# Performance work log

Hardware: AMD Instinct MI355X
Metric: run time of the kernel (lower is better)

The kernel has to match this reference:

```python
import jax, jax.numpy as jnp
import numpy as np

B, LB, LWIN, CODE, H, LAYERS = 256, 4, 128, 64, 256, 2


def _lstm_layer(xs, h0, c0, Wih, Whh, b):
    # xs: [T, B, in]; returns hs [T, B, H], final (h, c)
    WihT, WhhT = Wih.T, Whh.T
    def step(carry, x_t):
        h, c = carry
        gates = x_t @ WihT + h @ WhhT + b  # [B, 4H]
        i, f, g, o = jnp.split(gates, 4, axis=-1)  # PyTorch gate order i,f,g,o
        i, f, o = jax.nn.sigmoid(i), jax.nn.sigmoid(f), jax.nn.sigmoid(o)
        g = jnp.tanh(g)
        c_new = f * c + i * g
        h_new = o * jnp.tanh(c_new)
        return (h_new, c_new), h_new
    (h_n, c_n), hs = jax.lax.scan(step, (h0, c0), xs)
    return hs, h_n, c_n


def _run_stack(xs, states, params):
    # xs: [T, B, in]; states: list of (h, c) per layer
    new_states = []
    for (Wih, Whh, bih, bhh), (h0, c0) in zip(params, states):
        xs, h_n, c_n = _lstm_layer(xs, h0, c0, Wih, Whh, bih + bhh)
        new_states.append((h_n, c_n))
    return xs, new_states


def setup_inputs() -> dict:
    key = jax.random.key(0)
    ks = jax.random.split(key, 12)
    s = 0.05
    return {
        "x": jax.random.normal(ks[0], (B, LB, LWIN, CODE), jnp.float32),
        "targets": jax.random.normal(ks[1], (B, LWIN, CODE), jnp.float32),
        "Wih_0": jax.random.normal(ks[2], (4 * H, CODE), jnp.float32) * s,
        "Whh_0": jax.random.normal(ks[3], (4 * H, H), jnp.float32) * s,
        "bih_0": jax.random.normal(ks[4], (4 * H,), jnp.float32) * s,
        "bhh_0": jax.random.normal(ks[5], (4 * H,), jnp.float32) * s,
        "Wih_1": jax.random.normal(ks[6], (4 * H, H), jnp.float32) * s,
        "Whh_1": jax.random.normal(ks[7], (4 * H, H), jnp.float32) * s,
        "bih_1": jax.random.normal(ks[8], (4 * H,), jnp.float32) * s,
        "bhh_1": jax.random.normal(ks[9], (4 * H,), jnp.float32) * s,
        "fcW": jax.random.normal(ks[10], (CODE, H), jnp.float32) * s,
        "fcb": jax.random.normal(ks[11], (CODE,), jnp.float32) * s,
    }


def reference(x, targets, Wih_0, Whh_0, bih_0, bhh_0, Wih_1, Whh_1, bih_1, bhh_1, fcW, fcb):
    params = [(Wih_0, Whh_0, bih_0, bhh_0), (Wih_1, Whh_1, bih_1, bhh_1)]
    b = x.shape[0]
    xe = x.reshape(b, LB * LWIN, CODE)  # (B, look_back*l_win, code)
    zeros = jnp.zeros((b, H), x.dtype)
    states = [(zeros, zeros) for _ in range(LAYERS)]
    # Encoder pass to get (h_n, c_n)
    _, states = _run_stack(jnp.swapaxes(xe, 0, 1), states, params)
    # Teacher-forced decoder: inputs are known upfront
    dec_in = jnp.concatenate([xe[:, -1:, :], targets[:, :-1, :]], axis=1)  # (B, l_win, code)
    dec_hs, _ = _run_stack(jnp.swapaxes(dec_in, 0, 1), states, params)  # (l_win, B, H)
    out = jnp.einsum('tbh,ch->btc', dec_hs, fcW) + fcb  # (B, l_win, code)
    return out
```

## Files before the change

### kernel.cpp

```cpp
#include <hip/hip_runtime.h>
#include <math.h>

#define BATCH  256
#define CODE   64
#define HID    256
#define TSTEPS 640
#define NGRP   16

#define OFF_A0   0
#define OFF_A1   327680
#define OFF_BP0  851968
#define OFF_BP1  852992
#define OFF_HEX  854016
#define WS_FLOATS (OFF_HEX + 524288)

typedef __attribute__((ext_vector_type(8))) short  short8;
typedef __attribute__((ext_vector_type(4))) float  f32x4;
typedef __attribute__((ext_vector_type(4))) unsigned int u32x4;
typedef __attribute__((ext_vector_type(8))) __bf16 bf16x8;
typedef unsigned long long u64;

__device__ __forceinline__ f32x4 mfma16(short8 a, short8 b, f32x4 c) {
  return __builtin_amdgcn_mfma_f32_16x16x32_bf16(
      __builtin_bit_cast(bf16x8, a), __builtin_bit_cast(bf16x8, b), c, 0, 0, 0);
}
__device__ __forceinline__ unsigned short f2bf(float f) {
  union { float f; unsigned u; } v{f};
  unsigned r = v.u + 0x7fffu + ((v.u >> 16) & 1u);
  return (unsigned short)(r >> 16);
}
__device__ __forceinline__ float bf2f(unsigned short b) {
  union { unsigned u; float f; } v{(unsigned)b << 16};
  return v.f;
}
#define LOG2E 1.4426950408889634f
__device__ __forceinline__ float sigm(float x) {
  return __builtin_amdgcn_rcpf(1.0f + __builtin_amdgcn_exp2f(-x * LOG2E));
}
__device__ __forceinline__ float tanh_f(float x) {
  return 1.0f - 2.0f * __builtin_amdgcn_rcpf(1.0f + __builtin_amdgcn_exp2f(x * (2.0f * LOG2E)));
}

__global__ void setup_kernel(const float* __restrict__ Wih0, const float* __restrict__ Whh0,
                             const float* __restrict__ bih0, const float* __restrict__ bhh0,
                             const float* __restrict__ Wih1, const float* __restrict__ Whh1,
                             const float* __restrict__ bih1, const float* __restrict__ bhh1,
                             float* __restrict__ ws) {
  int i = blockIdx.x * 256 + threadIdx.x;
  unsigned short* u = (unsigned short*)ws;
  if (i < 327680) {
    int rt = i / 5120, r = i % 5120;
    int f = r >> 9, l = (r >> 3) & 63, j = r & 7;
    int p = rt * 16 + (l & 15);
    int orig = (p & 3) * 256 + (p >> 2);
    int k = f * 32 + ((l >> 4) << 3) + j;
    float w = (k < 64) ? Wih0[orig * 64 + k] : Whh0[orig * 256 + k - 64];
    unsigned short hi = f2bf(w);
    unsigned short lo = f2bf(w - bf2f(hi));
    int base = OFF_A0 * 2 + (((rt * 10 + f) * 2) * 64 + l) * 8 + j;
    u[base] = hi; u[base + 512] = lo;
    return;
  }
  i -= 327680;
  if (i < 524288) {
    int rt = i >> 13, r = i & 8191;
    int f = r >> 9, l = (r >> 3) & 63, j = r & 7;
    int p = rt * 16 + (l & 15);
    int orig = (p & 3) * 256 + (p >> 2);
    int k = f * 32 + ((l >> 4) << 3) + j;
    float w = (k < 256) ? Wih1[orig * 256 + k] : Whh1[orig * 256 + k - 256];
    unsigned short hi = f2bf(w);
    unsigned short lo = f2bf(w - bf2f(hi));
    int base = OFF_A1 * 2 + (((rt * 16 + f) * 2) * 64 + l) * 8 + j;
    u[base] = hi; u[base + 512] = lo;
    return;
  }
  i -= 524288;
  if (i < 2048) {
    int layer = i >> 10, p = i & 1023;
    int orig = (p & 3) * 256 + (p >> 2);
    ws[OFF_BP0 + i] = layer ? (bih1[orig] + bhh1[orig]) : (bih0[orig] + bhh0[orig]);
  }
}

__device__ __forceinline__ size_t qoff(int buf, int grp, int wgsrc, int layer, int uq, int b) {
  return (size_t)(((((buf * 16 + grp) * 16 + wgsrc) * 2 + layer) * 4 + uq) * 16 + b) * 16u;
}

__global__ __launch_bounds__(512, 2) void lstm_mfma(
    const float* __restrict__ x, const float* __restrict__ targets,
    const float* __restrict__ fcW, const float* __restrict__ fcb,
    float* __restrict__ ws, float* __restrict__ out) {
  __shared__ __align__(16) short Bx[2][64][8];
  __shared__ __align__(16) short Bh0[8][64][8];
  __shared__ __align__(16) short Bh1[8][64][8];
  __shared__ float fcw_s[64 * 257];

  const int t = threadIdx.x;
  const int blk = blockIdx.x;
  const int xcd = blk & 7, slot = blk >> 3;
  const int grp = xcd * 2 + (slot >> 4);
  const int wg  = slot & 15;

  const int w = t >> 6, l = t & 63, wl = w & 3;
  const bool isL0 = (w < 4);
  const int rt = wg * 4 + wl;

  char* hexb = (char*)(ws + OFF_HEX);

  for (int idx = t; idx < 64 * 256; idx += 512)
    fcw_s[(idx >> 8) * 257 + (idx & 255)] = fcW[idx];

  short8 Ah[16], Al[16];
  if (isL0) {
    const float* Ab = ws + OFF_A0 + rt * 5120;
#pragma unroll
    for (int f = 0; f < 10; ++f) {
      Ah[f] = *(const short8*)(Ab + ((f * 2 + 0) * 64 + l) * 4);
      Al[f] = *(const short8*)(Ab + ((f * 2 + 1) * 64 + l) * 4);
    }
  } else {
    const float* Ab = ws + OFF_A1 + rt * 8192;
#pragma unroll
    for (int f = 0; f < 16; ++f) {
      Ah[f] = *(const short8*)(Ab + ((f * 2 + 0) * 64 + l) * 4);
      Al[f] = *(const short8*)(Ab + ((f * 2 + 1) * 64 + l) * 4);
    }
  }
  const f32x4 bias = *(const f32x4*)(ws + (isL0 ? OFF_BP0 : OFF_BP1) + rt * 16 + ((l >> 4) << 2));
  const float fcb_r = fcb[4 * wg + (l & 3)];
  float cst = 0.0f;

  const int col = l & 15;
  const int k0 = (w << 5) + ((l >> 4) << 3);
  const int wgsrc = k0 >> 4, uq0 = (k0 & 15) >> 2;

  float4 xr0, xr1;
  auto load_x = [&](int s) {
    if (w < 2 && s < TSTEPS) {
      const float* src;
      if (s <= 512) {
        int ss = (s < 512) ? s : 511;
        src = x + ((size_t)(grp * 16 + col) * 512 + ss) * 64 + k0;
      } else {
        src = targets + ((size_t)(grp * 16 + col) * 128 + (s - 513)) * 64 + k0;
      }
      xr0 = *(const float4*)src;
      xr1 = *(const float4*)(src + 4);
    }
  };
  auto put_x = [&]() {
    if (w < 2) {
      short8 v;
      v[0] = (short)f2bf(xr0.x); v[1] = (short)f2bf(xr0.y);
      v[2] = (short)f2bf(xr0.z); v[3] = (short)f2bf(xr0.w);
      v[4] = (short)f2bf(xr1.x); v[5] = (short)f2bf(xr1.y);
      v[6] = (short)f2bf(xr1.z); v[7] = (short)f2bf(xr1.w);
      *(short8*)Bx[w][l] = v;
    }
  };

  *(u32x4*)&Bh0[w][l][0] = u32x4{0, 0, 0, 0};
  *(u32x4*)&Bh1[w][l][0] = u32x4{0, 0, 0, 0};
  load_x(0); put_x();
  __syncthreads();

  u32x4 q00, q01, q10, q11;

  for (int T = 0; T <= TSTEPS + 1; ++T) {
    float hh = 0.0f;
    const bool act = isL0 ? (T < TSTEPS) : (T >= 1 && T <= TSTEPS);
    if (act) {
      f32x4 aH0 = {0.f,0.f,0.f,0.f}, aH1 = {0.f,0.f,0.f,0.f};
      f32x4 aL0 = {0.f,0.f,0.f,0.f}, aL1 = {0.f,0.f,0.f,0.f};
      if (isL0) {
        {
          short8 b0 = *(const short8*)Bx[0][l];
          aH0 = mfma16(Ah[0], b0, aH0); aL0 = mfma16(Al[0], b0, aL0);
          short8 b1 = *(const short8*)Bx[1][l];
          aH1 = mfma16(Ah[1], b1, aH1); aL1 = mfma16(Al[1], b1, aL1);
        }
#pragma unroll
        for (int f = 2; f < 10; ++f) {
          short8 b = *(const short8*)Bh0[f - 2][l];
          if (f & 1) { aH1 = mfma16(Ah[f], b, aH1); aL1 = mfma16(Al[f], b, aL1); }
          else       { aH0 = mfma16(Ah[f], b, aH0); aL0 = mfma16(Al[f], b, aL0); }
        }
      } else {
#pragma unroll
        for (int f = 0; f < 8; ++f) {
          short8 b = *(const short8*)Bh0[f][l];
          if (f & 1) { aH1 = mfma16(Ah[f], b, aH1); aL1 = mfma16(Al[f], b, aL1); }
          else       { aH0 = mfma16(Ah[f], b, aH0); aL0 = mfma16(Al[f], b, aL0); }
        }
#pragma unroll
        for (int f = 8; f < 16; ++f) {
          short8 b = *(const short8*)Bh1[f - 8][l];
          if (f & 1) { aH1 = mfma16(Ah[f], b, aH1); aL1 = mfma16(Al[f], b, aL1); }
          else       { aH0 = mfma16(Ah[f], b, aH0); aL0 = mfma16(Al[f], b, aL0); }
        }
      }
      f32x4 s = aH0 + aH1 + aL0 + aL1 + bias;
      cst = sigm(s.y) * cst + sigm(s.x) * tanh_f(s.z);
      hh = sigm(s.w) * tanh_f(cst);
    }

    const unsigned tag = (unsigned)(T + 1);

    if (T <= TSTEPS) {
      unsigned bh = f2bf(hh);
      unsigned v0 = __shfl((int)bh, (l & 15));
      unsigned v1 = __shfl((int)bh, 16 + (l & 15));
      unsigned v2 = __shfl((int)bh, 32 + (l & 15));
      unsigned v3 = __shfl((int)bh, 48 + (l & 15));
      if (l < 16) {
        u32x4 ex = {tag, v0 | (v1 << 16), v2 | (v3 << 16), tag};
        char* pe = hexb + qoff(T & 1, grp, wg, isL0 ? 0 : 1, wl, l);
        asm volatile("global_store_dwordx4 %0, %1, off sc0 sc1"
                     :: "v"(pe), "v"(ex) : "memory");
      }
    }

    if (w < 2 && (T + 1) < TSTEPS) load_x(T + 1);

    if (w == 3 && T >= 514) {
      int d = T - 514;
      int code = 4 * wg + (l & 3), b = l >> 2;
      float acc = fcb_r;
#pragma unroll 4
      for (int k8 = 0; k8 < 32; ++k8) {
        short8 hv = *(const short8*)Bh1[k8 >> 2][(k8 & 3) * 16 + b];
#pragma unroll
        for (int j = 0; j < 8; ++j)
          acc = fmaf(fcw_s[code * 257 + k8 * 8 + j], bf2f((unsigned short)hv[j]), acc);
      }
      __builtin_nontemporal_store(acc, &out[(size_t)(grp * 16 + b) * 8192 + d * 64 + code]);
    }

    if (T <= TSTEPS) {
      char* pb = hexb + qoff(T & 1, grp, wgsrc, 0, uq0, col);
      while (true) {
        asm volatile(
            "global_load_dwordx4 %0, %4, off sc0 sc1\n\t"
            "global_load_dwordx4 %1, %4, off offset:256 sc0 sc1\n\t"
            "global_load_dwordx4 %2, %4, off offset:1024 sc0 sc1\n\t"
            "global_load_dwordx4 %3, %4, off offset:1280 sc0 sc1\n\t"
            "s_waitcnt vmcnt(0)"
            : "=v"(q00), "=v"(q01), "=v"(q10), "=v"(q11)
            : "v"(pb) : "memory");
        bool ok = (q00.x == tag) & (q00.w == tag) & (q01.x == tag) & (q01.w == tag) &
                  (q10.x == tag) & (q10.w == tag) & (q11.x == tag) & (q11.w == tag);
        if (__all(ok)) break;
      }
    }
    __syncthreads();

    if (T <= TSTEPS) {
      *(u32x4*)&Bh0[w][l][0] = u32x4{q00.y, q00.z, q01.y, q01.z};
      *(u32x4*)&Bh1[w][l][0] = u32x4{q10.y, q10.z, q11.y, q11.z};
      if ((T + 1) < TSTEPS) put_x();
    }
    __syncthreads();
  }
}

extern "C" void kernel_launch(void* const* d_in, const int* in_sizes, int n_in,
                              void* d_out, int out_size, void* d_ws, size_t ws_size,
                              hipStream_t stream) {
  const float* x       = (const float*)d_in[0];
  const float* targets = (const float*)d_in[1];
  const float* Wih0    = (const float*)d_in[2];
  const float* Whh0    = (const float*)d_in[3];
  const float* bih0    = (const float*)d_in[4];
  const float* bhh0    = (const float*)d_in[5];
  const float* Wih1    = (const float*)d_in[6];
  const float* Whh1    = (const float*)d_in[7];
  const float* bih1    = (const float*)d_in[8];
  const float* bhh1    = (const float*)d_in[9];
  const float* fcW     = (const float*)d_in[10];
  const float* fcb     = (const float*)d_in[11];
  float* ws = (float*)d_ws;
  float* o  = (float*)d_out;

  hipMemsetAsync((char*)d_ws + (size_t)OFF_HEX * 4, 0, (size_t)524288 * 4, stream);
  setup_kernel<<<3336, 256, 0, stream>>>(Wih0, Whh0, bih0, bhh0,
                                         Wih1, Whh1, bih1, bhh1, ws);
  lstm_mfma<<<256, 512, 0, stream>>>(x, targets, fcW, fcb, ws, o);
}
```

Before: 1.589 ms.

## Interleave two batch groups per block to overlap exchange latency with compute

Each workgroup now processes two independent batch groups in alternating phases, with double-buffered LDS for the x and h operands, and the grid is halved to 128 blocks. The goal is to hide the global-memory flag polling of one group's hidden-state exchange behind the MFMA and gate work of the other group. The loop is reordered so each phase first waits for the previous step's h, then computes, publishes, and prefetches. The FC projection also gets four independent accumulators to shorten its dependency chain. The XCD-aware mapping of groups to blocks is dropped, so a group's 16 blocks may now sit on different XCDs, and each block does twice the serial work per step.

```diff
diff --git a/kernel.cpp b/kernel.cpp
--- a/kernel.cpp
+++ b/kernel.cpp
@@ -5,7 +5,6 @@
 #define CODE   64
 #define HID    256
 #define TSTEPS 640
-#define NGRP   16
 
 #define OFF_A0   0
 #define OFF_A1   327680
@@ -91,16 +90,15 @@
     const float* __restrict__ x, const float* __restrict__ targets,
     const float* __restrict__ fcW, const float* __restrict__ fcb,
     float* __restrict__ ws, float* __restrict__ out) {
-  __shared__ __align__(16) short Bx[2][64][8];
-  __shared__ __align__(16) short Bh0[8][64][8];
-  __shared__ __align__(16) short Bh1[8][64][8];
+  __shared__ __align__(16) short Bx[2][2][64][8];
+  __shared__ __align__(16) short Bh0[2][8][64][8];
+  __shared__ __align__(16) short Bh1[2][8][64][8];
   __shared__ float fcw_s[64 * 257];
 
   const int t = threadIdx.x;
   const int blk = blockIdx.x;
-  const int xcd = blk & 7, slot = blk >> 3;
-  const int grp = xcd * 2 + (slot >> 4);
-  const int wg  = slot & 15;
+  const int pair = blk >> 4;
+  const int wg   = blk & 15;
 
   const int w = t >> 6, l = t & 63, wl = w & 3;
   const bool isL0 = (w < 4);
@@ -129,116 +127,37 @@
   }
   const f32x4 bias = *(const f32x4*)(ws + (isL0 ? OFF_BP0 : OFF_BP1) + rt * 16 + ((l >> 4) << 2));
   const float fcb_r = fcb[4 * wg + (l & 3)];
-  float cst = 0.0f;
+  float cstA = 0.0f, cstB = 0.0f;
 
   const int col = l & 15;
   const int k0 = (w << 5) + ((l >> 4) << 3);
   const int wgsrc = k0 >> 4, uq0 = (k0 & 15) >> 2;
 
-  float4 xr0, xr1;
-  auto load_x = [&](int s) {
+  auto load_x = [&](int g, int s, float4& xr0, float4& xr1) {
     if (w < 2 && s < TSTEPS) {
       const float* src;
       if (s <= 512) {
         int ss = (s < 512) ? s : 511;
-        src = x + ((size_t)(grp * 16 + col) * 512 + ss) * 64 + k0;
+        src = x + ((size_t)(g * 16 + col) * 512 + ss) * 64 + k0;
       } else {
-        src = targets + ((size_t)(grp * 16 + col) * 128 + (s - 513)) * 64 + k0;
+        src = targets + ((size_t)(g * 16 + col) * 128 + (s - 513)) * 64 + k0;
       }
       xr0 = *(const float4*)src;
       xr1 = *(const float4*)(src + 4);
     }
   };
-  auto put_x = [&]() {
-    if (w < 2) {
-      short8 v;
-      v[0] = (short)f2bf(xr0.x); v[1] = (short)f2bf(xr0.y);
-      v[2] = (short)f2bf(xr0.z); v[3] = (short)f2bf(xr0.w);
-      v[4] = (short)f2bf(xr1.x); v[5] = (short)f2bf(xr1.y);
-      v[6] = (short)f2bf(xr1.z); v[7] = (short)f2bf(xr1.w);
-      *(short8*)Bx[w][l] = v;
-    }
-  };
-
-  *(u32x4*)&Bh0[w][l][0] = u32x4{0, 0, 0, 0};
-  *(u32x4*)&Bh1[w][l][0] = u32x4{0, 0, 0, 0};
-  load_x(0); put_x();
-  __syncthreads();
-
-  u32x4 q00, q01, q10, q11;
-
-  for (int T = 0; T <= TSTEPS + 1; ++T) {
-    float hh = 0.0f;
-    const bool act = isL0 ? (T < TSTEPS) : (T >= 1 && T <= TSTEPS);
-    if (act) {
-      f32x4 aH0 = {0.f,0.f,0.f,0.f}, aH1 = {0.f,0.f,0.f,0.f};
-      f32x4 aL0 = {0.f,0.f,0.f,0.f}, aL1 = {0.f,0.f,0.f,0.f};
-      if (isL0) {
-        {
-          short8 b0 = *(const short8*)Bx[0][l];
-          aH0 = mfma16(Ah[0], b0, aH0); aL0 = mfma16(Al[0], b0, aL0);
-          short8 b1 = *(const short8*)Bx[1][l];
-          aH1 = mfma16(Ah[1], b1, aH1); aL1 = mfma16(Al[1], b1, aL1);
-        }
-#pragma unroll
-        for (int f = 2; f < 10; ++f) {
-          short8 b = *(const short8*)Bh0[f - 2][l];
-          if (f & 1) { aH1 = mfma16(Ah[f], b, aH1); aL1 = mfma16(Al[f], b, aL1); }
-          else       { aH0 = mfma16(Ah[f], b, aH0); aL0 = mfma16(Al[f], b, aL0); }
-        }
-      } else {
-#pragma unroll
-        for (int f = 0; f < 8; ++f) {
-          short8 b = *(const short8*)Bh0[f][l];
-          if (f & 1) { aH1 = mfma16(Ah[f], b, aH1); aL1 = mfma16(Al[f], b, aL1); }
-          else       { aH0 = mfma16(Ah[f], b, aH0); aL0 = mfma16(Al[f], b, aL0); }
-        }
-#pragma unroll
-        for (int f = 8; f < 16; ++f) {
-          short8 b = *(const short8*)Bh1[f - 8][l];
-          if (f & 1) { aH1 = mfma16(Ah[f], b, aH1); aL1 = mfma16(Al[f], b, aL1); }
-          else       { aH0 = mfma16(Ah[f], b, aH0); aL0 = mfma16(Al[f], b, aL0); }
-        }
-      }
-      f32x4 s = aH0 + aH1 + aL0 + aL1 + bias;
-      cst = sigm(s.y) * cst + sigm(s.x) * tanh_f(s.z);
-      hh = sigm(s.w) * tanh_f(cst);
-    }
-
-    const unsigned tag = (unsigned)(T + 1);
-
-    if (T <= TSTEPS) {
-      unsigned bh = f2bf(hh);
-      unsigned v0 = __shfl((int)bh, (l & 15));
-      unsigned v1 = __shfl((int)bh, 16 + (l & 15));
-      unsigned v2 = __shfl((int)bh, 32 + (l & 15));
-      unsigned v3 = __shfl((int)bh, 48 + (l & 15));
-      if (l < 16) {
-        u32x4 ex = {tag, v0 | (v1 << 16), v2 | (v3 << 16), tag};
-        char* pe = hexb + qoff(T & 1, grp, wg, isL0 ? 0 : 1, wl, l);
-        asm volatile("global_store_dwordx4 %0, %1, off sc0 sc1"
-                     :: "v"(pe), "v"(ex) : "memory");
-      }
-    }
-
-    if (w < 2 && (T + 1) < TSTEPS) load_x(T + 1);
-
-    if (w == 3 && T >= 514) {
-      int d = T - 514;
-      int code = 4 * wg + (l & 3), b = l >> 2;
-      float acc = fcb_r;
-#pragma unroll 4
-      for (int k8 = 0; k8 < 32; ++k8) {
-        short8 hv = *(const short8*)Bh1[k8 >> 2][(k8 & 3) * 16 + b];
-#pragma unroll
-        for (int j = 0; j < 8; ++j)
-          acc = fmaf(fcw_s[code * 257 + k8 * 8 + j], bf2f((unsigned short)hv[j]), acc);
-      }
-      __builtin_nontemporal_store(acc, &out[(size_t)(grp * 16 + b) * 8192 + d * 64 + code]);
-    }
-
-    if (T <= TSTEPS) {
-      char* pb = hexb + qoff(T & 1, grp, wgsrc, 0, uq0, col);
+
+  float4 xA0, xA1, xB0, xB1;
+  load_x(2 * pair + 0, 0, xA0, xA1);
+  load_x(2 * pair + 1, 0, xB0, xB1);
+
+  auto phase = [&](const int s, const int T, float& cst, float4& xr0, float4& xr1) {
+    const int g = 2 * pair + s;
+    const unsigned tag = (unsigned)T;
+    u32x4 q00, q01, q10, q11;
+
+    {
+      char* pb = hexb + qoff((T + 1) & 1, g, wgsrc, 0, uq0, col);
       while (true) {
         asm volatile(
             "global_load_dwordx4 %0, %4, off sc0 sc1\n\t"
@@ -253,14 +172,99 @@
         if (__all(ok)) break;
       }
     }
+
+    *(u32x4*)&Bh0[s][w][l][0] = u32x4{q00.y, q00.z, q01.y, q01.z};
+    *(u32x4*)&Bh1[s][w][l][0] = u32x4{q10.y, q10.z, q11.y, q11.z};
+    if (w < 2 && T < TSTEPS) {
+      short8 v;
+      v[0] = (short)f2bf(xr0.x); v[1] = (short)f2bf(xr0.y);
+      v[2] = (short)f2bf(xr0.z); v[3] = (short)f2bf(xr0.w);
+      v[4] = (short)f2bf(xr1.x); v[5] = (short)f2bf(xr1.y);
+      v[6] = (short)f2bf(xr1.z); v[7] = (short)f2bf(xr1.w);
+      *(short8*)Bx[s][w][l] = v;
+    }
     __syncthreads();
 
+    float hh = 0.0f;
+    const bool act = isL0 ? (T < TSTEPS) : (T >= 1 && T <= TSTEPS);
+    if (act) {
+      f32x4 aH0 = {0.f,0.f,0.f,0.f}, aH1 = {0.f,0.f,0.f,0.f};
+      f32x4 aL0 = {0.f,0.f,0.f,0.f}, aL1 = {0.f,0.f,0.f,0.f};
+      if (isL0) {
+        {
+          short8 b0 = *(const short8*)Bx[s][0][l];
+          aH0 = mfma16(Ah[0], b0, aH0); aL0 = mfma16(Al[0], b0, aL0);
+          short8 b1 = *(const short8*)Bx[s][1][l];
+          aH1 = mfma16(Ah[1], b1, aH1); aL1 = mfma16(Al[1], b1, aL1);
+        }
+#pragma unroll
+        for (int f = 2; f < 10; ++f) {
+          short8 b = *(const short8*)Bh0[s][f - 2][l];
+          if (f & 1) { aH1 = mfma16(Ah[f], b, aH1); aL1 = mfma16(Al[f], b, aL1); }
+          else       { aH0 = mfma16(Ah[f], b, aH0); aL0 = mfma16(Al[f], b, aL0); }
+        }
+      } else {
+#pragma unroll
+        for (int f = 0; f < 8; ++f) {
+          short8 b = *(const short8*)Bh0[s][f][l];
+          if (f & 1) { aH1 = mfma16(Ah[f], b, aH1); aL1 = mfma16(Al[f], b, aL1); }
+          else       { aH0 = mfma16(Ah[f], b, aH0); aL0 = mfma16(Al[f], b, aL0); }
+        }
+#pragma unroll
+        for (int f = 8; f < 16; ++f) {
+          short8 b = *(const short8*)Bh1[s][f - 8][l];
+          if (f & 1) { aH1 = mfma16(Ah[f], b, aH1); aL1 = mfma16(Al[f], b, aL1); }
+          else       { aH0 = mfma16(Ah[f], b, aH0); aL0 = mfma16(Al[f], b, aL0); }
+        }
+      }
+      f32x4 sv = aH0 + aH1 + aL0 + aL1 + bias;
+      cst = sigm(sv.y) * cst + sigm(sv.x) * tanh_f(sv.z);
+      hh = sigm(sv.w) * tanh_f(cst);
+    }
+
     if (T <= TSTEPS) {
-      *(u32x4*)&Bh0[w][l][0] = u32x4{q00.y, q00.z, q01.y, q01.z};
-      *(u32x4*)&Bh1[w][l][0] = u32x4{q10.y, q10.z, q11.y, q11.z};
-      if ((T + 1) < TSTEPS) put_x();
-    }
-    __syncthreads();
+      unsigned bh = f2bf(hh);
+      unsigned v0 = __shfl((int)bh, (l & 15));
+      unsigned v1 = __shfl((int)bh, 16 + (l & 15));
+      unsigned v2 = __shfl((int)bh, 32 + (l & 15));
+      unsigned v3 = __shfl((int)bh, 48 + (l & 15));
+      if (l < 16) {
+        u32x4 ex = {(unsigned)(T + 1), v0 | (v1 << 16), v2 | (v3 << 16), (unsigned)(T + 1)};
+        char* pe = hexb + qoff(T & 1, g, wg, isL0 ? 0 : 1, wl, l);
+        asm volatile("global_store_dwordx4 %0, %1, off sc0 sc1"
+                     :: "v"(pe), "v"(ex) : "memory");
+      }
+    }
+
+    if (w < 2 && (T + 1) < TSTEPS) load_x(g, T + 1, xr0, xr1);
+
+    if (w == 3 && T >= 514) {
+      int d = T - 514;
+      int code = 4 * wg + (l & 3), b = l >> 2;
+      float a0 = fcb_r, a1 = 0.f, a2 = 0.f, a3 = 0.f;
+#pragma unroll
+      for (int kq = 0; kq < 8; ++kq) {
+        short8 h0v = *(const short8*)Bh1[s][kq][0 * 16 + b];
+        short8 h1v = *(const short8*)Bh1[s][kq][1 * 16 + b];
+        short8 h2v = *(const short8*)Bh1[s][kq][2 * 16 + b];
+        short8 h3v = *(const short8*)Bh1[s][kq][3 * 16 + b];
+        const float* fw = fcw_s + code * 257 + kq * 32;
+#pragma unroll
+        for (int j = 0; j < 8; ++j) {
+          a0 = fmaf(fw[j],      bf2f((unsigned short)h0v[j]), a0);
+          a1 = fmaf(fw[8 + j],  bf2f((unsigned short)h1v[j]), a1);
+          a2 = fmaf(fw[16 + j], bf2f((unsigned short)h2v[j]), a2);
+          a3 = fmaf(fw[24 + j], bf2f((unsigned short)h3v[j]), a3);
+        }
+      }
+      float acc = (a0 + a1) + (a2 + a3);
+      __builtin_nontemporal_store(acc, &out[(size_t)(g * 16 + b) * 8192 + d * 64 + code]);
+    }
+  };
+
+  for (int T = 0; T <= TSTEPS + 1; ++T) {
+    phase(0, T, cstA, xA0, xA1);
+    phase(1, T, cstB, xB0, xB1);
   }
 }
 
@@ -285,5 +289,5 @@
   hipMemsetAsync((char*)d_ws + (size_t)OFF_HEX * 4, 0, (size_t)524288 * 4, stream);
   setup_kernel<<<3336, 256, 0, stream>>>(Wih0, Whh0, bih0, bhh0,
                                          Wih1, Whh1, bih1, bhh1, ws);
-  lstm_mfma<<<256, 512, 0, stream>>>(x, targets, fcW, fcb, ws, o);
-}
+  lstm_mfma<<<128, 512, 0, stream>>>(x, targets, fcW, fcb, ws, o);
+}
```

Result: slower. 3.323 ms (+109.2%).

## Double-buffer LDS recurrent state to drop a barrier per timestep

Applied to the files above, without the earlier changes.

Adds ping-pong copies of the x and hidden-state LDS buffers so each step writes the next step's operands into the other buffer, which removes one __syncthreads per timestep. It also adds a spin phase that polls a single slot before the full four-slot poll, and splits the FC projection into four independent accumulators to shorten the dependency chain. The cost is twice the LDS for these buffers and more polling loads on the cross-workgroup exchange.

```diff
diff --git a/kernel.cpp b/kernel.cpp
--- a/kernel.cpp
+++ b/kernel.cpp
@@ -5,7 +5,6 @@
 #define CODE   64
 #define HID    256
 #define TSTEPS 640
-#define NGRP   16
 
 #define OFF_A0   0
 #define OFF_A1   327680
@@ -91,9 +90,9 @@
     const float* __restrict__ x, const float* __restrict__ targets,
     const float* __restrict__ fcW, const float* __restrict__ fcb,
     float* __restrict__ ws, float* __restrict__ out) {
-  __shared__ __align__(16) short Bx[2][64][8];
-  __shared__ __align__(16) short Bh0[8][64][8];
-  __shared__ __align__(16) short Bh1[8][64][8];
+  __shared__ __align__(16) short Bx[2][2][64][8];
+  __shared__ __align__(16) short Bh0[2][8][64][8];
+  __shared__ __align__(16) short Bh1[2][8][64][8];
   __shared__ float fcw_s[64 * 257];
 
   const int t = threadIdx.x;
@@ -149,25 +148,25 @@
       xr1 = *(const float4*)(src + 4);
     }
   };
-  auto put_x = [&]() {
+  auto put_x = [&](int p) {
     if (w < 2) {
       short8 v;
       v[0] = (short)f2bf(xr0.x); v[1] = (short)f2bf(xr0.y);
       v[2] = (short)f2bf(xr0.z); v[3] = (short)f2bf(xr0.w);
       v[4] = (short)f2bf(xr1.x); v[5] = (short)f2bf(xr1.y);
       v[6] = (short)f2bf(xr1.z); v[7] = (short)f2bf(xr1.w);
-      *(short8*)Bx[w][l] = v;
+      *(short8*)Bx[p][w][l] = v;
     }
   };
 
-  *(u32x4*)&Bh0[w][l][0] = u32x4{0, 0, 0, 0};
-  *(u32x4*)&Bh1[w][l][0] = u32x4{0, 0, 0, 0};
-  load_x(0); put_x();
+  *(u32x4*)&Bh0[0][w][l][0] = u32x4{0, 0, 0, 0};
+  *(u32x4*)&Bh1[0][w][l][0] = u32x4{0, 0, 0, 0};
+  load_x(0); put_x(0);
   __syncthreads();
 
-  u32x4 q00, q01, q10, q11;
-
   for (int T = 0; T <= TSTEPS + 1; ++T) {
+    const int p = T & 1;
+
     float hh = 0.0f;
     const bool act = isL0 ? (T < TSTEPS) : (T >= 1 && T <= TSTEPS);
     if (act) {
@@ -175,27 +174,27 @@
       f32x4 aL0 = {0.f,0.f,0.f,0.f}, aL1 = {0.f,0.f,0.f,0.f};
       if (isL0) {
         {
-          short8 b0 = *(const short8*)Bx[0][l];
+          short8 b0 = *(const short8*)Bx[p][0][l];
           aH0 = mfma16(Ah[0], b0, aH0); aL0 = mfma16(Al[0], b0, aL0);
-          short8 b1 = *(const short8*)Bx[1][l];
+          short8 b1 = *(const short8*)Bx[p][1][l];
           aH1 = mfma16(Ah[1], b1, aH1); aL1 = mfma16(Al[1], b1, aL1);
         }
 #pragma unroll
         for (int f = 2; f < 10; ++f) {
-          short8 b = *(const short8*)Bh0[f - 2][l];
+          short8 b = *(const short8*)Bh0[p][f - 2][l];
           if (f & 1) { aH1 = mfma16(Ah[f], b, aH1); aL1 = mfma16(Al[f], b, aL1); }
           else       { aH0 = mfma16(Ah[f], b, aH0); aL0 = mfma16(Al[f], b, aL0); }
         }
       } else {
 #pragma unroll
         for (int f = 0; f < 8; ++f) {
-          short8 b = *(const short8*)Bh0[f][l];
+          short8 b = *(const short8*)Bh0[p][f][l];
           if (f & 1) { aH1 = mfma16(Ah[f], b, aH1); aL1 = mfma16(Al[f], b, aL1); }
           else       { aH0 = mfma16(Ah[f], b, aH0); aL0 = mfma16(Al[f], b, aL0); }
         }
 #pragma unroll
         for (int f = 8; f < 16; ++f) {
-          short8 b = *(const short8*)Bh1[f - 8][l];
+          short8 b = *(const short8*)Bh1[p][f - 8][l];
           if (f & 1) { aH1 = mfma16(Ah[f], b, aH1); aL1 = mfma16(Al[f], b, aL1); }
           else       { aH0 = mfma16(Ah[f], b, aH0); aL0 = mfma16(Al[f], b, aL0); }
         }
@@ -215,7 +214,7 @@
       unsigned v3 = __shfl((int)bh, 48 + (l & 15));
       if (l < 16) {
         u32x4 ex = {tag, v0 | (v1 << 16), v2 | (v3 << 16), tag};
-        char* pe = hexb + qoff(T & 1, grp, wg, isL0 ? 0 : 1, wl, l);
+        char* pe = hexb + qoff(p, grp, wg, isL0 ? 0 : 1, wl, l);
         asm volatile("global_store_dwordx4 %0, %1, off sc0 sc1"
                      :: "v"(pe), "v"(ex) : "memory");
       }
@@ -226,19 +225,38 @@
     if (w == 3 && T >= 514) {
       int d = T - 514;
       int code = 4 * wg + (l & 3), b = l >> 2;
-      float acc = fcb_r;
-#pragma unroll 4
-      for (int k8 = 0; k8 < 32; ++k8) {
-        short8 hv = *(const short8*)Bh1[k8 >> 2][(k8 & 3) * 16 + b];
-#pragma unroll
-        for (int j = 0; j < 8; ++j)
-          acc = fmaf(fcw_s[code * 257 + k8 * 8 + j], bf2f((unsigned short)hv[j]), acc);
-      }
+      float a0 = fcb_r, a1 = 0.f, a2 = 0.f, a3 = 0.f;
+#pragma unroll
+      for (int kq = 0; kq < 8; ++kq) {
+        short8 h0v = *(const short8*)Bh1[p][kq][0 * 16 + b];
+        short8 h1v = *(const short8*)Bh1[p][kq][1 * 16 + b];
+        short8 h2v = *(const short8*)Bh1[p][kq][2 * 16 + b];
+        short8 h3v = *(const short8*)Bh1[p][kq][3 * 16 + b];
+        const float* fw = fcw_s + code * 257 + kq * 32;
+#pragma unroll
+        for (int j = 0; j < 8; ++j) {
+          a0 = fmaf(fw[j],      bf2f((unsigned short)h0v[j]), a0);
+          a1 = fmaf(fw[8 + j],  bf2f((unsigned short)h1v[j]), a1);
+          a2 = fmaf(fw[16 + j], bf2f((unsigned short)h2v[j]), a2);
+          a3 = fmaf(fw[24 + j], bf2f((unsigned short)h3v[j]), a3);
+        }
+      }
+      float acc = (a0 + a1) + (a2 + a3);
       __builtin_nontemporal_store(acc, &out[(size_t)(grp * 16 + b) * 8192 + d * 64 + code]);
     }
 
     if (T <= TSTEPS) {
-      char* pb = hexb + qoff(T & 1, grp, wgsrc, 0, uq0, col);
+      char* pb = hexb + qoff(p, grp, wgsrc, 0, uq0, col);
+      u32x4 q00, q01, q10, q11;
+      {
+        u32x4 qs;
+        char* ps = pb + 1280;
+        do {
+          asm volatile("global_load_dwordx4 %0, %1, off sc0 sc1\n\t"
+                       "s_waitcnt vmcnt(0)"
+                       : "=v"(qs) : "v"(ps) : "memory");
+        } while (!__all((qs.x == tag) & (qs.w == tag)));
+      }
       while (true) {
         asm volatile(
             "global_load_dwordx4 %0, %4, off sc0 sc1\n\t"
@@ -252,13 +270,9 @@
                   (q10.x == tag) & (q10.w == tag) & (q11.x == tag) & (q11.w == tag);
         if (__all(ok)) break;
       }
-    }
-    __syncthreads();
-
-    if (T <= TSTEPS) {
-      *(u32x4*)&Bh0[w][l][0] = u32x4{q00.y, q00.z, q01.y, q01.z};
-      *(u32x4*)&Bh1[w][l][0] = u32x4{q10.y, q10.z, q11.y, q11.z};
-      if ((T + 1) < TSTEPS) put_x();
+      *(u32x4*)&Bh0[p ^ 1][w][l][0] = u32x4{q00.y, q00.z, q01.y, q01.z};
+      *(u32x4*)&Bh1[p ^ 1][w][l][0] = u32x4{q10.y, q10.z, q11.y, q11.z};
+      if ((T + 1) < TSTEPS) put_x(p ^ 1);
     }
     __syncthreads();
   }
```

New measurement: 1.666 ms. 1.05x slower.
